# Optimization experiments

Measured on AMD Instinct MI355X. Metric: run time of the kernel, lower is better.

Reference implementation:

```python
import jax, jax.numpy as jnp
import numpy as np

N, E, F, FE, H, R = 100000, 3200000, 2, 7, 64, 500
BN_EPS = 1e-5
LEAKY_SLOPE = 0.01


def _bn(h, g, b):
    # BatchNorm1d in training mode: batch statistics over the node axis
    m = h.mean(0)
    v = h.var(0)
    return (h - m) * jax.lax.rsqrt(v + BN_EPS) * g + b


def _gine_conv(x, src, dst, edge_attr, eps, el_w, el_b, w1, b1, g, bt, w2, b2):
    # message: relu(x_j + Lin(edge_attr)); aggregate: scatter-add at dst
    msg = jax.nn.relu(x[src] + edge_attr @ el_w + el_b)          # [E, d]
    agg = jax.ops.segment_sum(msg, dst, num_segments=N)          # [N, d]
    h = (1.0 + eps) * x + agg
    # nn: Linear -> BN -> ReLU -> Linear -> ReLU
    h = jax.nn.relu(_bn(h @ w1 + b1, g, bt))
    return jax.nn.relu(h @ w2 + b2)


def setup_inputs() -> dict:
    key = jax.random.key(0)
    ks = jax.random.split(key, 16)
    r = lambda k, s, sc=0.1: jax.random.normal(k, s, dtype=jnp.float32) * sc
    return {
        "x": jax.random.normal(ks[0], (N, F), dtype=jnp.float32),
        "edge_attr": jax.random.normal(ks[1], (E, FE), dtype=jnp.float32),
        "edge_index": jax.random.randint(ks[2], (2, E), 0, N),
        "epoch": 1,
        "eps1": jnp.zeros((), jnp.float32),
        "el1_w": r(ks[3], (FE, F)), "el1_b": jnp.zeros((F,), jnp.float32),
        "n1_w1": r(ks[4], (F, H)), "n1_b1": jnp.zeros((H,), jnp.float32),
        "n1_g": jnp.ones((H,), jnp.float32), "n1_bt": jnp.zeros((H,), jnp.float32),
        "n1_w2": r(ks[5], (H, H)), "n1_b2": jnp.zeros((H,), jnp.float32),
        "eps2": jnp.zeros((), jnp.float32),
        "el2_w": r(ks[6], (FE, H)), "el2_b": jnp.zeros((H,), jnp.float32),
        "n2_w1": r(ks[7], (H, H)), "n2_b1": jnp.zeros((H,), jnp.float32),
        "n2_g": jnp.ones((H,), jnp.float32), "n2_bt": jnp.zeros((H,), jnp.float32),
        "n2_w2": r(ks[8], (H, H)), "n2_b2": jnp.zeros((H,), jnp.float32),
        "reg_w": r(ks[9], (H, R)), "reg_b": jnp.zeros((R,), jnp.float32),
        "end_w": r(ks[10], (R, 1)), "end_b": jnp.zeros((1,), jnp.float32),
    }


def reference(x, edge_attr, edge_index, epoch,
              eps1, el1_w, el1_b, n1_w1, n1_b1, n1_g, n1_bt, n1_w2, n1_b2,
              eps2, el2_w, el2_b, n2_w1, n2_b1, n2_g, n2_bt, n2_w2, n2_b2,
              reg_w, reg_b, end_w, end_b):
    src, dst = edge_index[0], edge_index[1]
    out = _gine_conv(x, src, dst, edge_attr, eps1, el1_w, el1_b,
                     n1_w1, n1_b1, n1_g, n1_bt, n1_w2, n1_b2)
    for _ in range(3 - 1):  # num_layers=3, shared conv2 weights
        out = _gine_conv(out, src, dst, edge_attr, eps2, el2_w, el2_b,
                         n2_w1, n2_b1, n2_g, n2_bt, n2_w2, n2_b2)
    # dropout p=0.0 -> identity; epoch only resets dropout, no effect here
    out = out @ reg_w + reg_b
    out = jnp.where(out >= 0, out, LEAKY_SLOPE * out)  # LeakyReLU
    out = out @ end_w + end_b                            # [N, 1]
    return out
```

## Files before the change

### kernel.cpp

```cpp
#include <hip/hip_runtime.h>
#include <hip/hip_fp16.h>

#define NN 100000
#define NE 3200000

__device__ inline unsigned pkh(float a, float b) {
  __half2 h;
  h.x = __float2half(a);
  h.y = __float2half(b);
  unsigned u;
  __builtin_memcpy(&u, &h, 4);
  return u;
}
__device__ inline float2 uph(unsigned u) {
  __half2 h;
  __builtin_memcpy(&h, &u, 4);
  return __half22float2(h);
}
__device__ inline float h1f(unsigned short v) {
  __half h;
  __builtin_memcpy(&h, &v, 2);
  return __half2float(h);
}
__device__ inline unsigned short f1h(float f) {
  __half h = __float2half(f);
  unsigned short u;
  __builtin_memcpy(&u, &h, 2);
  return u;
}

__global__ __launch_bounds__(256) void count_kernel(const int* __restrict__ dst,
                                                    int* __restrict__ cnt) {
  int stride = gridDim.x * 256;
  for (int e = blockIdx.x * 256 + threadIdx.x; e < NE; e += stride)
    atomicAdd(&cnt[dst[e]], 1);
}

__global__ __launch_bounds__(1024) void scan_kernel(const int* __restrict__ cnt,
                                                    int* __restrict__ rowptr,
                                                    int* __restrict__ ofs) {
  __shared__ int bsum[1024];
  int tid = threadIdx.x;
  const int CH = (NN + 1023) / 1024;
  int lo = tid * CH, hi = lo + CH < NN ? lo + CH : NN;
  if (lo > NN) lo = NN;
  if (hi < lo) hi = lo;
  int s = 0;
  for (int i = lo; i < hi; i++) s += cnt[i];
  bsum[tid] = s;
  __syncthreads();
  for (int off = 1; off < 1024; off <<= 1) {
    int v = bsum[tid];
    int u = (tid >= off) ? bsum[tid - off] : 0;
    __syncthreads();
    bsum[tid] = v + u;
    __syncthreads();
  }
  int pre = (tid == 0) ? 0 : bsum[tid - 1];
  for (int i = lo; i < hi; i++) {
    int cv = cnt[i];
    rowptr[i] = pre;
    ofs[i] = pre;
    pre += cv;
  }
  if (tid == 1023) rowptr[NN] = pre;
}

__global__ __launch_bounds__(256) void scatter2h_kernel(
    const int* __restrict__ src, const int* __restrict__ dst,
    const float* __restrict__ ea, int* __restrict__ ofs,
    uint4* __restrict__ erec, int* __restrict__ esrc,
    const float* __restrict__ x, const float* __restrict__ elw,
    const float* __restrict__ elb, float* __restrict__ msg1) {
  float w0[7], w1r[7];
#pragma unroll
  for (int k = 0; k < 7; k++) { w0[k] = elw[k * 2]; w1r[k] = elw[k * 2 + 1]; }
  float b0 = elb[0], b1 = elb[1];
  int stride = gridDim.x * 256;
  for (int e = blockIdx.x * 256 + threadIdx.x; e < NE; e += stride) {
    int sn = src[e];
    int pos = atomicAdd(&ofs[dst[e]], 1);
    float av[7];
#pragma unroll
    for (int k = 0; k < 7; k++) av[k] = ea[e * 7 + k];
    uint4 r;
    r.x = pkh(av[0], av[1]);
    r.y = pkh(av[2], av[3]);
    r.z = pkh(av[4], av[5]);
    r.w = pkh(av[6], 0.f);
    erec[pos] = r;
    esrc[pos] = sn;
    float m0 = b0, m1 = b1;
#pragma unroll
    for (int k = 0; k < 7; k++) {
      m0 = fmaf(av[k], w0[k], m0);
      m1 = fmaf(av[k], w1r[k], m1);
    }
    m0 = fmaxf(m0 + x[sn * 2 + 0], 0.f);
    m1 = fmaxf(m1 + x[sn * 2 + 1], 0.f);
    float2 mv; mv.x = m0; mv.y = m1;
    ((float2*)msg1)[pos] = mv;
  }
}

__global__ __launch_bounds__(256) void scatter1_kernel(
    const int* __restrict__ dst, int* __restrict__ ofs, int* __restrict__ eid_s) {
  int stride = gridDim.x * 256;
  for (int e = blockIdx.x * 256 + threadIdx.x; e < NE; e += stride) {
    int pos = atomicAdd(&ofs[dst[e]], 1);
    eid_s[pos] = e;
  }
}

__global__ __launch_bounds__(256) void l1sum_kernel(
    const int* __restrict__ rowptr, const float* __restrict__ msg1,
    float* __restrict__ agg) {
  int stride = gridDim.x * 256;
  for (int n = blockIdx.x * 256 + threadIdx.x; n < NN; n += stride) {
    int r0 = rowptr[n], r1 = rowptr[n + 1];
    float a0 = 0.f, a1 = 0.f;
    const float2* mp = (const float2*)msg1;
    for (int i = r0; i < r1; i++) {
      float2 v = mp[i];
      a0 += v.x;
      a1 += v.y;
    }
    agg[n * 2 + 0] = a0;
    agg[n * 2 + 1] = a1;
  }
}

__global__ __launch_bounds__(256) void l1agg_kernel(
    const int* __restrict__ rowptr, const int* __restrict__ eid_s,
    const int* __restrict__ src, const float* __restrict__ ea,
    const float* __restrict__ x, const float* __restrict__ elw,
    const float* __restrict__ elb, float* __restrict__ agg) {
  float w0[7], w1r[7];
#pragma unroll
  for (int k = 0; k < 7; k++) { w0[k] = elw[k * 2]; w1r[k] = elw[k * 2 + 1]; }
  float b0 = elb[0], b1 = elb[1];
  int stride = gridDim.x * 256;
  for (int n = blockIdx.x * 256 + threadIdx.x; n < NN; n += stride) {
    int r0 = rowptr[n], r1 = rowptr[n + 1];
    float a0 = 0.f, a1 = 0.f;
    for (int i = r0; i < r1; i++) {
      int e = eid_s[i];
      int sn = src[e];
      float m0 = b0, m1 = b1;
#pragma unroll
      for (int k = 0; k < 7; k++) {
        float a = ea[e * 7 + k];
        m0 = fmaf(a, w0[k], m0);
        m1 = fmaf(a, w1r[k], m1);
      }
      m0 = fmaxf(m0 + x[sn * 2 + 0], 0.f);
      m1 = fmaxf(m1 + x[sn * 2 + 1], 0.f);
      a0 += m0; a1 += m1;
    }
    agg[n * 2 + 0] = a0;
    agg[n * 2 + 1] = a1;
  }
}

#define PROJH(m, u) do { \
  float2 q0 = uph((u).x), q1 = uph((u).y), q2 = uph((u).z), q3 = uph((u).w); \
  m = bel; \
  m = fmaf(q0.x, wel[0], m); m = fmaf(q0.y, wel[1], m); \
  m = fmaf(q1.x, wel[2], m); m = fmaf(q1.y, wel[3], m); \
  m = fmaf(q2.x, wel[4], m); m = fmaf(q2.y, wel[5], m); \
  m = fmaf(q3.x, wel[6], m); } while (0)

__global__ __launch_bounds__(256) void gine64h_kernel(
    const int* __restrict__ rowptr, const uint4* __restrict__ erec,
    const int* __restrict__ esrc, const float* __restrict__ xin,
    const unsigned short* __restrict__ xh, const float* __restrict__ elw,
    const float* __restrict__ elb, const float* __restrict__ w1,
    const float* __restrict__ b1, const float* __restrict__ eps_p,
    float* __restrict__ tbuf, float* __restrict__ stats) {
  __shared__ float wl[64 * 64];
  __shared__ float hb[4][64];
  __shared__ float red[256];
  int tid = threadIdx.x, lane = tid & 63, wv = tid >> 6;
  for (int i2 = tid; i2 < 64 * 64; i2 += 256) wl[i2] = w1[i2];
  float wel[7];
#pragma unroll
  for (int k = 0; k < 7; k++) wel[k] = elw[k * 64 + lane];
  float bel = elb[lane], b1c = b1[lane];
  float ep = 1.0f + *eps_p;
  float s = 0.f, ss = 0.f;
  __syncthreads();
  const unsigned short* xl = xh + lane;
  int nw = gridDim.x * 4;
  for (int n = blockIdx.x * 4 + wv; n < NN; n += nw) {
    int r0 = rowptr[n], r1 = rowptr[n + 1];
    float acc = 0.f;
    int i = r0;
    int rem = r1 - r0;
    if (rem >= 4) {
      uint4 u0 = erec[i], u1 = erec[i + 1], u2 = erec[i + 2], u3 = erec[i + 3];
      int s0 = esrc[i], s1 = esrc[i + 1], s2 = esrc[i + 2], s3 = esrc[i + 3];
      while (true) {
        float g0 = h1f(xl[s0 * 64]);
        float g1 = h1f(xl[s1 * 64]);
        float g2 = h1f(xl[s2 * 64]);
        float g3 = h1f(xl[s3 * 64]);
        i += 4; rem -= 4;
        bool more = rem >= 4;
        int ip = more ? i : r0;
        uint4 v0 = erec[ip], v1 = erec[ip + 1], v2 = erec[ip + 2], v3 = erec[ip + 3];
        int t0 = esrc[ip], t1 = esrc[ip + 1], t2 = esrc[ip + 2], t3 = esrc[ip + 3];
        float m0, m1, m2, m3;
        PROJH(m0, u0); PROJH(m1, u1); PROJH(m2, u2); PROJH(m3, u3);
        acc += fmaxf(m0 + g0, 0.f);
        acc += fmaxf(m1 + g1, 0.f);
        acc += fmaxf(m2 + g2, 0.f);
        acc += fmaxf(m3 + g3, 0.f);
        u0 = v0; u1 = v1; u2 = v2; u3 = v3;
        s0 = t0; s1 = t1; s2 = t2; s3 = t3;
        if (!more) break;
      }
    }
    for (; i < r1; i++) {
      uint4 u = erec[i];
      int sn = esrc[i];
      float m;
      PROJH(m, u);
      m += h1f(xl[sn * 64]);
      acc += fmaxf(m, 0.f);
    }
    float h = ep * xin[n * 64 + lane] + acc;
    hb[wv][lane] = h;
    float t = b1c;
#pragma unroll
    for (int k = 0; k < 64; k++) t = fmaf(hb[wv][k], wl[k * 64 + lane], t);
    tbuf[n * 64 + lane] = t;
    s += t;
    ss += t * t;
  }
  double* dsum = (double*)stats;
  red[tid] = s;
  __syncthreads();
  if (tid < 64) unsafeAtomicAdd(&dsum[tid], (double)(red[tid] + red[tid + 64] + red[tid + 128] + red[tid + 192]));
  __syncthreads();
  red[tid] = ss;
  __syncthreads();
  if (tid < 64) unsafeAtomicAdd(&dsum[64 + tid], (double)(red[tid] + red[tid + 64] + red[tid + 128] + red[tid + 192]));
}

__global__ __launch_bounds__(256) void gine64s_kernel(
    const int* __restrict__ rowptr, const int* __restrict__ eid_s,
    const int* __restrict__ src, const float* __restrict__ ea,
    const float* __restrict__ xin, const float* __restrict__ elw,
    const float* __restrict__ elb, const float* __restrict__ w1,
    const float* __restrict__ b1, const float* __restrict__ eps_p,
    float* __restrict__ tbuf, float* __restrict__ stats) {
  __shared__ float wl[64 * 64];
  __shared__ float hb[4][64];
  __shared__ float red[256];
  int tid = threadIdx.x, lane = tid & 63, wv = tid >> 6;
  for (int i = tid; i < 64 * 64; i += 256) wl[i] = w1[i];
  float wel[7];
#pragma unroll
  for (int k = 0; k < 7; k++) wel[k] = elw[k * 64 + lane];
  float bel = elb[lane], b1c = b1[lane];
  float ep = 1.0f + *eps_p;
  float s = 0.f, ss = 0.f;
  __syncthreads();
  int nw = gridDim.x * 4;
  for (int n = blockIdx.x * 4 + wv; n < NN; n += nw) {
    int r0 = rowptr[n], r1 = rowptr[n + 1];
    float acc = 0.f;
    for (int i = r0; i < r1; i++) {
      int e = eid_s[i];
      int sn = src[e];
      float m = bel;
#pragma unroll
      for (int k = 0; k < 7; k++) m = fmaf(ea[e * 7 + k], wel[k], m);
      m += xin[sn * 64 + lane];
      acc += fmaxf(m, 0.f);
    }
    float h = ep * xin[n * 64 + lane] + acc;
    hb[wv][lane] = h;
    float t = b1c;
#pragma unroll
    for (int k = 0; k < 64; k++) t = fmaf(hb[wv][k], wl[k * 64 + lane], t);
    tbuf[n * 64 + lane] = t;
    s += t;
    ss += t * t;
  }
  double* dsum = (double*)stats;
  red[tid] = s;
  __syncthreads();
  if (tid < 64) unsafeAtomicAdd(&dsum[tid], (double)(red[tid] + red[tid + 64] + red[tid + 128] + red[tid + 192]));
  __syncthreads();
  red[tid] = ss;
  __syncthreads();
  if (tid < 64) unsafeAtomicAdd(&dsum[64 + tid], (double)(red[tid] + red[tid + 64] + red[tid + 128] + red[tid + 192]));
}

__global__ __launch_bounds__(256) void edge1_kernel(
    const float* __restrict__ x, const float* __restrict__ ea,
    const int* __restrict__ src, const int* __restrict__ dst,
    const float* __restrict__ elw, const float* __restrict__ elb,
    float* __restrict__ agg) {
  float w0[7], w1[7];
#pragma unroll
  for (int k = 0; k < 7; k++) { w0[k] = elw[k * 2]; w1[k] = elw[k * 2 + 1]; }
  float b0 = elb[0], b1 = elb[1];
  int stride = gridDim.x * 256;
  for (int e = blockIdx.x * 256 + threadIdx.x; e < NE; e += stride) {
    int s = src[e], d = dst[e];
    float m0 = b0, m1 = b1;
#pragma unroll
    for (int k = 0; k < 7; k++) {
      float a = ea[e * 7 + k];
      m0 = fmaf(a, w0[k], m0);
      m1 = fmaf(a, w1[k], m1);
    }
    m0 = fmaxf(m0 + x[s * 2 + 0], 0.f);
    m1 = fmaxf(m1 + x[s * 2 + 1], 0.f);
    unsafeAtomicAdd(&agg[d * 2 + 0], m0);
    unsafeAtomicAdd(&agg[d * 2 + 1], m1);
  }
}

__global__ __launch_bounds__(256) void edge64_kernel(
    const float* __restrict__ xin, const float* __restrict__ ea,
    const int* __restrict__ src, const int* __restrict__ dst,
    const float* __restrict__ elw, const float* __restrict__ elb,
    float* __restrict__ agg) {
  int lane = threadIdx.x & 63;
  int wid = (blockIdx.x * 256 + threadIdx.x) >> 6;
  int nw = (gridDim.x * 256) >> 6;
  float w[7];
#pragma unroll
  for (int k = 0; k < 7; k++) w[k] = elw[k * 64 + lane];
  float b = elb[lane];
  for (int e = wid; e < NE; e += nw) {
    int eu = __builtin_amdgcn_readfirstlane(e);
    int s = src[eu];
    int d = dst[eu];
    float m = b;
#pragma unroll
    for (int k = 0; k < 7; k++) m = fmaf(ea[eu * 7 + k], w[k], m);
    m += xin[s * 64 + lane];
    m = fmaxf(m, 0.f);
    unsafeAtomicAdd(&agg[d * 64 + lane], m);
  }
}

__global__ __launch_bounds__(256) void nodeA64_kernel(
    const float* __restrict__ xin, float* __restrict__ tbuf,
    const float* __restrict__ w1, const float* __restrict__ b1,
    const float* __restrict__ eps_p, float* __restrict__ stats) {
  __shared__ float wl[64 * 64];
  __shared__ float hbuf[4][64];
  __shared__ float red[256];
  int tid = threadIdx.x;
  int c = tid & 63, nl = tid >> 6;
  for (int i = tid; i < 64 * 64; i += 256) wl[i] = w1[i];
  float ep = 1.0f + *eps_p;
  float bc = b1[c];
  float s = 0.f, ss = 0.f;
  __syncthreads();
  for (int n0 = blockIdx.x * 4; n0 < NN; n0 += gridDim.x * 4) {
    int n = n0 + nl;
    bool valid = n < NN;
    float h = 0.f;
    if (valid) h = ep * xin[n * 64 + c] + tbuf[n * 64 + c];
    hbuf[nl][c] = h;
    __syncthreads();
    if (valid) {
      float t = bc;
#pragma unroll
      for (int k = 0; k < 64; k++) t = fmaf(hbuf[nl][k], wl[k * 64 + c], t);
      tbuf[n * 64 + c] = t;
      s += t;
      ss += t * t;
    }
    __syncthreads();
  }
  double* dsum = (double*)stats;
  red[tid] = s;
  __syncthreads();
  if (tid < 64) unsafeAtomicAdd(&dsum[tid], (double)(red[tid] + red[tid + 64] + red[tid + 128] + red[tid + 192]));
  __syncthreads();
  red[tid] = ss;
  __syncthreads();
  if (tid < 64) unsafeAtomicAdd(&dsum[64 + tid], (double)(red[tid] + red[tid + 64] + red[tid + 128] + red[tid + 192]));
}

__global__ __launch_bounds__(256) void nodeA2_kernel(
    const float* __restrict__ x, const float* __restrict__ agg1,
    float* __restrict__ tbuf, const float* __restrict__ w1,
    const float* __restrict__ b1, const float* __restrict__ eps_p,
    float* __restrict__ stats) {
  __shared__ float red[256];
  int tid = threadIdx.x;
  int c = tid & 63, nl = tid >> 6;
  float wa = w1[c], wb = w1[64 + c], bc = b1[c];
  float ep = 1.0f + *eps_p;
  float s = 0.f, ss = 0.f;
  for (int n0 = blockIdx.x * 4; n0 < NN; n0 += gridDim.x * 4) {
    int n = n0 + nl;
    if (n < NN) {
      float h0 = ep * x[n * 2 + 0] + agg1[n * 2 + 0];
      float h1 = ep * x[n * 2 + 1] + agg1[n * 2 + 1];
      float t = fmaf(h1, wb, fmaf(h0, wa, bc));
      tbuf[n * 64 + c] = t;
      s += t;
      ss += t * t;
    }
  }
  double* dsum = (double*)stats;
  red[tid] = s;
  __syncthreads();
  if (tid < 64) unsafeAtomicAdd(&dsum[tid], (double)(red[tid] + red[tid + 64] + red[tid + 128] + red[tid + 192]));
  __syncthreads();
  red[tid] = ss;
  __syncthreads();
  if (tid < 64) unsafeAtomicAdd(&dsum[64 + tid], (double)(red[tid] + red[tid + 64] + red[tid + 128] + red[tid + 192]));
}

__global__ __launch_bounds__(256) void nodeB_kernel(
    const float* __restrict__ tin, float* __restrict__ outb,
    const float* __restrict__ w2, const float* __restrict__ b2,
    const float* __restrict__ stats, const float* __restrict__ g,
    const float* __restrict__ bt, unsigned short* __restrict__ xh) {
  __shared__ float wl[64 * 64];
  __shared__ float ubuf[4][64];
  __shared__ float scsh[128];
  int tid = threadIdx.x;
  int c = tid & 63, nl = tid >> 6;
  for (int i = tid; i < 64 * 64; i += 256) wl[i] = w2[i];
  if (tid < 64) {
    const double* ds = (const double*)stats;
    double m = ds[tid] / (double)NN;
    double v = ds[64 + tid] / (double)NN - m * m;
    float sc = g[tid] * (float)(1.0 / sqrt(v + 1e-5));
    scsh[tid] = sc;
    scsh[64 + tid] = bt[tid] - (float)m * sc;
  }
  float bc = b2[c];
  __syncthreads();
  float scale = scsh[c], shift = scsh[64 + c];
  for (int n0 = blockIdx.x * 4; n0 < NN; n0 += gridDim.x * 4) {
    int n = n0 + nl;
    bool valid = n < NN;
    float u = 0.f;
    if (valid) {
      float t = tin[n * 64 + c];
      u = fmaxf(fmaf(t, scale, shift), 0.f);
    }
    ubuf[nl][c] = u;
    __syncthreads();
    if (valid) {
      float o = bc;
#pragma unroll
      for (int k = 0; k < 64; k++) o = fmaf(ubuf[nl][k], wl[k * 64 + c], o);
      o = fmaxf(o, 0.f);
      outb[n * 64 + c] = o;
      if (xh) xh[n * 64 + c] = f1h(o);
    }
    __syncthreads();
  }
}

__global__ __launch_bounds__(256) void final_kernel(
    const float* __restrict__ xin, const float* __restrict__ regw,
    const float* __restrict__ regb, const float* __restrict__ endw,
    const float* __restrict__ endb, float* __restrict__ out) {
  __shared__ float wl[64 * 128];
  __shared__ float eb[256];
  int tid = threadIdx.x;
  int node = blockIdx.x * 256 + tid;
  bool valid = node < NN;
  float xr[64];
  if (valid) {
    const float4* xp = (const float4*)(xin + node * 64);
#pragma unroll
    for (int k4 = 0; k4 < 16; k4++) {
      float4 v = xp[k4];
      xr[k4 * 4 + 0] = v.x; xr[k4 * 4 + 1] = v.y;
      xr[k4 * 4 + 2] = v.z; xr[k4 * 4 + 3] = v.w;
    }
  }
  float y = 0.f;
  for (int ch = 0; ch < 4; ch++) {
    int j0 = ch * 125;
    __syncthreads();
    for (int idx = tid; idx < 64 * 125; idx += 256) {
      int k = idx / 125;
      int jl = idx - k * 125;
      wl[k * 128 + jl] = regw[k * 500 + j0 + jl];
    }
    if (tid < 125) { eb[tid] = regb[j0 + tid]; eb[128 + tid] = endw[j0 + tid]; }
    __syncthreads();
    if (valid) {
      int jl = 0;
      for (; jl + 4 <= 125; jl += 4) {
        float t0 = eb[jl], t1 = eb[jl + 1], t2 = eb[jl + 2], t3 = eb[jl + 3];
#pragma unroll
        for (int k = 0; k < 64; k++) {
          float4 w4 = *(const float4*)&wl[k * 128 + jl];
          float xv = xr[k];
          t0 = fmaf(xv, w4.x, t0);
          t1 = fmaf(xv, w4.y, t1);
          t2 = fmaf(xv, w4.z, t2);
          t3 = fmaf(xv, w4.w, t3);
        }
        t0 = t0 >= 0.f ? t0 : 0.01f * t0;
        t1 = t1 >= 0.f ? t1 : 0.01f * t1;
        t2 = t2 >= 0.f ? t2 : 0.01f * t2;
        t3 = t3 >= 0.f ? t3 : 0.01f * t3;
        y += t0 * eb[128 + jl] + t1 * eb[128 + jl + 1] + t2 * eb[128 + jl + 2] + t3 * eb[128 + jl + 3];
      }
      {
        float t = eb[124];
#pragma unroll
        for (int k = 0; k < 64; k++) t = fmaf(xr[k], wl[k * 128 + 124], t);
        t = t >= 0.f ? t : 0.01f * t;
        y += t * eb[128 + 124];
      }
    }
  }
  if (valid) out[node] = y + endb[0];
}

extern "C" void kernel_launch(void* const* d_in, const int* in_sizes, int n_in,
                              void* d_out, int out_size, void* d_ws, size_t ws_size,
                              hipStream_t stream) {
  const float* x    = (const float*)d_in[0];
  const float* ea   = (const float*)d_in[1];
  const int*   ei   = (const int*)d_in[2];
  const float* eps1 = (const float*)d_in[4];
  const float* el1w = (const float*)d_in[5];
  const float* el1b = (const float*)d_in[6];
  const float* n1w1 = (const float*)d_in[7];
  const float* n1b1 = (const float*)d_in[8];
  const float* n1g  = (const float*)d_in[9];
  const float* n1bt = (const float*)d_in[10];
  const float* n1w2 = (const float*)d_in[11];
  const float* n1b2 = (const float*)d_in[12];
  const float* eps2 = (const float*)d_in[13];
  const float* el2w = (const float*)d_in[14];
  const float* el2b = (const float*)d_in[15];
  const float* n2w1 = (const float*)d_in[16];
  const float* n2b1 = (const float*)d_in[17];
  const float* n2g  = (const float*)d_in[18];
  const float* n2bt = (const float*)d_in[19];
  const float* n2w2 = (const float*)d_in[20];
  const float* n2b2 = (const float*)d_in[21];
  const float* regw = (const float*)d_in[22];
  const float* regb = (const float*)d_in[23];
  const float* endw = (const float*)d_in[24];
  const float* endb = (const float*)d_in[25];
  const int* srcp = ei;
  const int* dstp = ei + NE;

  const size_t o_stats  = 0;
  const size_t o_cnt    = 768;
  const size_t o_rowptr = 100768;
  const size_t o_buf0   = 200832;
  const size_t o_buf1   = 6600832;
  const size_t o_xh     = 13000832;
  const size_t o_agg1   = 16200832;
  const size_t o_edat   = 16400832;
  const size_t o_srcs   = 29200832;
  const size_t needA2 = (o_srcs + (size_t)NE) * 4;
  const size_t needA1 = (o_edat + (size_t)NE) * 4;
  const size_t needB  = (2 * 6600000 + 384) * 4;

  float* wsf = (float*)d_ws;

  if (ws_size >= needA1) {
    const bool packed = ws_size >= needA2;
    float* stats0 = wsf + o_stats;
    float* stats1 = wsf + o_stats + 256;
    float* stats2 = wsf + o_stats + 512;
    int* cnt     = (int*)(wsf + o_cnt);
    int* rowptr  = (int*)(wsf + o_rowptr);
    float* buf0  = wsf + o_buf0;
    float* buf1  = wsf + o_buf1;
    unsigned short* xh = (unsigned short*)(wsf + o_xh);
    float* agg1  = wsf + o_agg1;
    uint4* erec  = (uint4*)(wsf + o_edat);
    int* esrc    = (int*)(wsf + o_srcs);
    float* msg1  = buf0;

    hipMemsetAsync(wsf, 0, (768 + NN) * sizeof(float), stream);

    count_kernel<<<4096, 256, 0, stream>>>(dstp, cnt);
    scan_kernel<<<1, 1024, 0, stream>>>(cnt, rowptr, cnt);
    if (packed)
      scatter2h_kernel<<<4096, 256, 0, stream>>>(srcp, dstp, ea, cnt, erec, esrc,
                                                 x, el1w, el1b, msg1);
    else
      scatter1_kernel<<<4096, 256, 0, stream>>>(dstp, cnt, (int*)(wsf + o_edat));

    if (packed)
      l1sum_kernel<<<391, 256, 0, stream>>>(rowptr, msg1, agg1);
    else
      l1agg_kernel<<<391, 256, 0, stream>>>(rowptr, (const int*)(wsf + o_edat),
                                            srcp, ea, x, el1w, el1b, agg1);
    nodeA2_kernel<<<2048, 256, 0, stream>>>(x, agg1, buf1, n1w1, n1b1, eps1, stats0);
    nodeB_kernel<<<2048, 256, 0, stream>>>(buf1, buf1, n1w2, n1b2, stats0,
                                           n1g, n1bt, packed ? xh : nullptr);

    if (packed) {
      gine64h_kernel<<<4096, 256, 0, stream>>>(rowptr, erec, esrc, buf1, xh,
                                               el2w, el2b, n2w1, n2b1, eps2,
                                               buf0, stats1);
      nodeB_kernel<<<2048, 256, 0, stream>>>(buf0, buf0, n2w2, n2b2, stats1,
                                             n2g, n2bt, xh);
      gine64h_kernel<<<4096, 256, 0, stream>>>(rowptr, erec, esrc, buf0, xh,
                                               el2w, el2b, n2w1, n2b1, eps2,
                                               buf1, stats2);
      nodeB_kernel<<<2048, 256, 0, stream>>>(buf1, buf1, n2w2, n2b2, stats2,
                                             n2g, n2bt, nullptr);
      final_kernel<<<(NN + 255) / 256, 256, 0, stream>>>(buf1, regw, regb, endw,
                                                         endb, (float*)d_out);
    } else {
      float* cur = buf1;
      float* wrk = buf0;
      float* sl[2] = {stats1, stats2};
      for (int l = 0; l < 2; l++) {
        gine64s_kernel<<<4096, 256, 0, stream>>>(rowptr, (const int*)(wsf + o_edat),
                                                 srcp, ea, cur, el2w, el2b, n2w1,
                                                 n2b1, eps2, wrk, sl[l]);
        nodeB_kernel<<<2048, 256, 0, stream>>>(wrk, wrk, n2w2, n2b2, sl[l],
                                               n2g, n2bt, nullptr);
        float* tmp = cur; cur = wrk; wrk = tmp;
      }
      final_kernel<<<(NN + 255) / 256, 256, 0, stream>>>(cur, regw, regb, endw,
                                                         endb, (float*)d_out);
    }
    return;
  }

  if (ws_size < needB) return;
  const size_t BUF = 6600000;
  float* buf0 = (float*)d_ws;
  float* buf1 = buf0 + BUF;
  float* stats = buf1 + BUF;

  float* t1 = buf1;
  float* agg1 = buf1 + NN * 64;
  hipMemsetAsync(agg1, 0, NN * 2 * sizeof(float), stream);
  hipMemsetAsync(stats, 0, 128 * sizeof(double), stream);
  edge1_kernel<<<2048, 256, 0, stream>>>(x, ea, srcp, dstp, el1w, el1b, agg1);
  nodeA2_kernel<<<2048, 256, 0, stream>>>(x, agg1, t1, n1w1, n1b1, eps1, stats);
  nodeB_kernel<<<2048, 256, 0, stream>>>(t1, buf1, n1w2, n1b2, stats, n1g, n1bt,
                                         nullptr);

  float* cur = buf1;
  float* wrk = buf0;
  for (int l = 0; l < 2; l++) {
    hipMemsetAsync(wrk, 0, NN * 64 * sizeof(float), stream);
    hipMemsetAsync(stats, 0, 128 * sizeof(double), stream);
    edge64_kernel<<<2048, 256, 0, stream>>>(cur, ea, srcp, dstp, el2w, el2b, wrk);
    nodeA64_kernel<<<2048, 256, 0, stream>>>(cur, wrk, n2w1, n2b1, eps2, stats);
    nodeB_kernel<<<2048, 256, 0, stream>>>(wrk, wrk, n2w2, n2b2, stats, n2g, n2bt,
                                           nullptr);
    float* tmp = cur; cur = wrk; wrk = tmp;
  }

  final_kernel<<<(NN + 255) / 256, 256, 0, stream>>>(cur, regw, regb, endw, endb,
                                                     (float*)d_out);
}
```

Measured before the change: 1.346 ms.

## Two-pass binned CSR sort with fused layer-1 aggregation via atomics

Replaces the single random-scatter edge sort with a two-pass scheme. Edges are first scattered into coarse bins of 128 destination nodes into a packed staging buffer, with the source id split across spare half bits and a byte array. A per-bin kernel then does the fine scatter inside a small, cache-friendly region and accumulates the layer-1 messages straight into agg1 with float atomics, which removes the msg1 buffer and the l1sum pass. This adds an extra pass over the edge data and float atomics, so the layer-1 sums become order-dependent, and the packing relies on node ids fitting in 17 bits.

```diff
diff --git a/kernel.cpp b/kernel.cpp
--- a/kernel.cpp
+++ b/kernel.cpp
@@ -3,6 +3,7 @@
 
 #define NN 100000
 #define NE 3200000
+#define NBINS 782
 
 __device__ inline unsigned pkh(float a, float b) {
   __half2 h;
@@ -66,40 +67,72 @@
   if (tid == 1023) rowptr[NN] = pre;
 }
 
-__global__ __launch_bounds__(256) void scatter2h_kernel(
+__global__ __launch_bounds__(1024) void binit_kernel(const int* __restrict__ rowptr,
+                                                     int* __restrict__ binofs) {
+  int t = threadIdx.x;
+  if (t < NBINS) binofs[t] = rowptr[t * 128];
+}
+
+__global__ __launch_bounds__(256) void binscat_kernel(
     const int* __restrict__ src, const int* __restrict__ dst,
-    const float* __restrict__ ea, int* __restrict__ ofs,
-    uint4* __restrict__ erec, int* __restrict__ esrc,
-    const float* __restrict__ x, const float* __restrict__ elw,
-    const float* __restrict__ elb, float* __restrict__ msg1) {
-  float w0[7], w1r[7];
-#pragma unroll
-  for (int k = 0; k < 7; k++) { w0[k] = elw[k * 2]; w1r[k] = elw[k * 2 + 1]; }
-  float b0 = elb[0], b1 = elb[1];
+    const float* __restrict__ ea, int* __restrict__ binofs,
+    uint4* __restrict__ stageA, unsigned char* __restrict__ stageB) {
   int stride = gridDim.x * 256;
   for (int e = blockIdx.x * 256 + threadIdx.x; e < NE; e += stride) {
     int sn = src[e];
-    int pos = atomicAdd(&ofs[dst[e]], 1);
+    int dn = dst[e];
+    int pos = atomicAdd(&binofs[dn >> 7], 1);
     float av[7];
 #pragma unroll
     for (int k = 0; k < 7; k++) av[k] = ea[e * 7 + k];
+    unsigned extra = ((unsigned)(dn & 127) << 9) | ((unsigned)sn >> 8);
     uint4 r;
     r.x = pkh(av[0], av[1]);
     r.y = pkh(av[2], av[3]);
     r.z = pkh(av[4], av[5]);
-    r.w = pkh(av[6], 0.f);
-    erec[pos] = r;
+    r.w = (unsigned)f1h(av[6]) | (extra << 16);
+    stageA[pos] = r;
+    stageB[pos] = (unsigned char)(sn & 255);
+  }
+}
+
+__global__ __launch_bounds__(256) void binsort_kernel(
+    const int* __restrict__ rowptr, const uint4* __restrict__ stageA,
+    const unsigned char* __restrict__ stageB, int* __restrict__ ofs,
+    uint4* __restrict__ erec, int* __restrict__ esrc,
+    const float* __restrict__ x, const float* __restrict__ elw,
+    const float* __restrict__ elb, float* __restrict__ agg1) {
+  float w0[7], w1r[7];
+#pragma unroll
+  for (int k = 0; k < 7; k++) { w0[k] = elw[k * 2]; w1r[k] = elw[k * 2 + 1]; }
+  float b0 = elb[0], b1 = elb[1];
+  int b = blockIdx.x;
+  int nhi = (b + 1) * 128;
+  if (nhi > NN) nhi = NN;
+  int r0 = rowptr[b * 128], r1 = rowptr[nhi];
+  int base = b << 7;
+  for (int i = r0 + threadIdx.x; i < r1; i += 256) {
+    uint4 u = stageA[i];
+    unsigned extra = u.w >> 16;
+    int sn = (int)(((extra & 0x1FF) << 8) | (unsigned)stageB[i]);
+    int dn = base + (int)(extra >> 9);
+    int pos = atomicAdd(&ofs[dn], 1);
+    erec[pos] = u;
     esrc[pos] = sn;
+    float2 q0 = uph(u.x), q1 = uph(u.y), q2 = uph(u.z);
+    float e6 = h1f((unsigned short)(u.w & 0xFFFF));
     float m0 = b0, m1 = b1;
-#pragma unroll
-    for (int k = 0; k < 7; k++) {
-      m0 = fmaf(av[k], w0[k], m0);
-      m1 = fmaf(av[k], w1r[k], m1);
-    }
+    m0 = fmaf(q0.x, w0[0], m0); m1 = fmaf(q0.x, w1r[0], m1);
+    m0 = fmaf(q0.y, w0[1], m0); m1 = fmaf(q0.y, w1r[1], m1);
+    m0 = fmaf(q1.x, w0[2], m0); m1 = fmaf(q1.x, w1r[2], m1);
+    m0 = fmaf(q1.y, w0[3], m0); m1 = fmaf(q1.y, w1r[3], m1);
+    m0 = fmaf(q2.x, w0[4], m0); m1 = fmaf(q2.x, w1r[4], m1);
+    m0 = fmaf(q2.y, w0[5], m0); m1 = fmaf(q2.y, w1r[5], m1);
+    m0 = fmaf(e6, w0[6], m0);   m1 = fmaf(e6, w1r[6], m1);
     m0 = fmaxf(m0 + x[sn * 2 + 0], 0.f);
     m1 = fmaxf(m1 + x[sn * 2 + 1], 0.f);
-    float2 mv; mv.x = m0; mv.y = m1;
-    ((float2*)msg1)[pos] = mv;
+    unsafeAtomicAdd(&agg1[dn * 2 + 0], m0);
+    unsafeAtomicAdd(&agg1[dn * 2 + 1], m1);
   }
 }
 
@@ -109,24 +142,6 @@
   for (int e = blockIdx.x * 256 + threadIdx.x; e < NE; e += stride) {
     int pos = atomicAdd(&ofs[dst[e]], 1);
     eid_s[pos] = e;
-  }
-}
-
-__global__ __launch_bounds__(256) void l1sum_kernel(
-    const int* __restrict__ rowptr, const float* __restrict__ msg1,
-    float* __restrict__ agg) {
-  int stride = gridDim.x * 256;
-  for (int n = blockIdx.x * 256 + threadIdx.x; n < NN; n += stride) {
-    int r0 = rowptr[n], r1 = rowptr[n + 1];
-    float a0 = 0.f, a1 = 0.f;
-    const float2* mp = (const float2*)msg1;
-    for (int i = r0; i < r1; i++) {
-      float2 v = mp[i];
-      a0 += v.x;
-      a1 += v.y;
-    }
-    agg[n * 2 + 0] = a0;
-    agg[n * 2 + 1] = a1;
   }
 }
 
@@ -559,16 +574,17 @@
   const int* dstp = ei + NE;
 
   const size_t o_stats  = 0;
-  const size_t o_cnt    = 768;
-  const size_t o_rowptr = 100768;
-  const size_t o_buf0   = 200832;
-  const size_t o_buf1   = 6600832;
-  const size_t o_xh     = 13000832;
-  const size_t o_agg1   = 16200832;
-  const size_t o_edat   = 16400832;
-  const size_t o_srcs   = 29200832;
-  const size_t needA2 = (o_srcs + (size_t)NE) * 4;
-  const size_t needA1 = (o_edat + (size_t)NE) * 4;
+  const size_t o_agg1   = 768;
+  const size_t o_cnt    = 200768;
+  const size_t o_binofs = 300768;
+  const size_t o_rowptr = 301568;
+  const size_t o_buf0   = 401600;
+  const size_t o_buf1   = 6801600;
+  const size_t o_xh     = 13201600;
+  const size_t o_erec   = 16401600;
+  const size_t o_esrc   = 29201600;
+  const size_t needA2 = (o_esrc + (size_t)NE) * 4;
+  const size_t needA1 = (o_erec + (size_t)NE) * 4;
   const size_t needB  = (2 * 6600000 + 384) * 4;
 
   float* wsf = (float*)d_ws;
@@ -578,31 +594,34 @@
     float* stats0 = wsf + o_stats;
     float* stats1 = wsf + o_stats + 256;
     float* stats2 = wsf + o_stats + 512;
+    float* agg1  = wsf + o_agg1;
     int* cnt     = (int*)(wsf + o_cnt);
+    int* binofs  = (int*)(wsf + o_binofs);
     int* rowptr  = (int*)(wsf + o_rowptr);
     float* buf0  = wsf + o_buf0;
     float* buf1  = wsf + o_buf1;
     unsigned short* xh = (unsigned short*)(wsf + o_xh);
-    float* agg1  = wsf + o_agg1;
-    uint4* erec  = (uint4*)(wsf + o_edat);
-    int* esrc    = (int*)(wsf + o_srcs);
-    float* msg1  = buf0;
-
-    hipMemsetAsync(wsf, 0, (768 + NN) * sizeof(float), stream);
+    uint4* erec  = (uint4*)(wsf + o_erec);
+    int* esrc    = (int*)(wsf + o_esrc);
+    uint4* stageA = (uint4*)(wsf + o_buf0);
+    unsigned char* stageB = (unsigned char*)(wsf + o_xh);
+
+    hipMemsetAsync(wsf, 0, (o_binofs) * sizeof(float), stream);
 
     count_kernel<<<4096, 256, 0, stream>>>(dstp, cnt);
     scan_kernel<<<1, 1024, 0, stream>>>(cnt, rowptr, cnt);
-    if (packed)
-      scatter2h_kernel<<<4096, 256, 0, stream>>>(srcp, dstp, ea, cnt, erec, esrc,
-                                                 x, el1w, el1b, msg1);
-    else
-      scatter1_kernel<<<4096, 256, 0, stream>>>(dstp, cnt, (int*)(wsf + o_edat));
-
-    if (packed)
-      l1sum_kernel<<<391, 256, 0, stream>>>(rowptr, msg1, agg1);
-    else
-      l1agg_kernel<<<391, 256, 0, stream>>>(rowptr, (const int*)(wsf + o_edat),
+    if (packed) {
+      binit_kernel<<<1, 1024, 0, stream>>>(rowptr, binofs);
+      binscat_kernel<<<4096, 256, 0, stream>>>(srcp, dstp, ea, binofs,
+                                               stageA, stageB);
+      binsort_kernel<<<NBINS, 256, 0, stream>>>(rowptr, stageA, stageB, cnt,
+                                                erec, esrc, x, el1w, el1b, agg1);
+    } else {
+      scatter1_kernel<<<4096, 256, 0, stream>>>(dstp, cnt, (int*)(wsf + o_erec));
+      l1agg_kernel<<<391, 256, 0, stream>>>(rowptr, (const int*)(wsf + o_erec),
                                             srcp, ea, x, el1w, el1b, agg1);
+    }
+
     nodeA2_kernel<<<2048, 256, 0, stream>>>(x, agg1, buf1, n1w1, n1b1, eps1, stats0);
     nodeB_kernel<<<2048, 256, 0, stream>>>(buf1, buf1, n1w2, n1b2, stats0,
                                            n1g, n1bt, packed ? xh : nullptr);
@@ -625,7 +644,7 @@
       float* wrk = buf0;
       float* sl[2] = {stats1, stats2};
       for (int l = 0; l < 2; l++) {
-        gine64s_kernel<<<4096, 256, 0, stream>>>(rowptr, (const int*)(wsf + o_edat),
+        gine64s_kernel<<<4096, 256, 0, stream>>>(rowptr, (const int*)(wsf + o_erec),
                                                  srcp, ea, cur, el2w, el2b, n2w1,
                                                  n2b1, eps2, wrk, sl[l]);
         nodeB_kernel<<<2048, 256, 0, stream>>>(wrk, wrk, n2w2, n2b2, sl[l],
```

Measured after the change: 2.164 ms. 60.7% more time.

## Pack source index into edge record and fuse layer-1 aggregation via atomics

Applied to the files above, without the earlier changes.

The 17-bit source node index is now packed into the spare half of the last word of each 16-byte edge record, taking the low mantissa bit of the seventh attribute. This removes the separate esrc array and its loads in both 64-wide GINE layers. Layer-1 messages are now atomically added straight into agg1 in the scatter kernel, which drops the msg1 buffer and the l1sum pass. The cost is float atomic contention on 200k addresses, a nondeterministic summation order, and a tiny precision loss in edge attribute 6.

```diff
diff --git a/kernel.cpp b/kernel.cpp
--- a/kernel.cpp
+++ b/kernel.cpp
@@ -66,12 +66,12 @@
   if (tid == 1023) rowptr[NN] = pre;
 }
 
-__global__ __launch_bounds__(256) void scatter2h_kernel(
+__global__ __launch_bounds__(256) void scatter2c_kernel(
     const int* __restrict__ src, const int* __restrict__ dst,
     const float* __restrict__ ea, int* __restrict__ ofs,
-    uint4* __restrict__ erec, int* __restrict__ esrc,
-    const float* __restrict__ x, const float* __restrict__ elw,
-    const float* __restrict__ elb, float* __restrict__ msg1) {
+    uint4* __restrict__ erec, const float* __restrict__ x,
+    const float* __restrict__ elw, const float* __restrict__ elb,
+    float* __restrict__ agg1) {
   float w0[7], w1r[7];
 #pragma unroll
   for (int k = 0; k < 7; k++) { w0[k] = elw[k * 2]; w1r[k] = elw[k * 2 + 1]; }
@@ -79,7 +79,8 @@
   int stride = gridDim.x * 256;
   for (int e = blockIdx.x * 256 + threadIdx.x; e < NE; e += stride) {
     int sn = src[e];
-    int pos = atomicAdd(&ofs[dst[e]], 1);
+    int dn = dst[e];
+    int pos = atomicAdd(&ofs[dn], 1);
     float av[7];
 #pragma unroll
     for (int k = 0; k < 7; k++) av[k] = ea[e * 7 + k];
@@ -87,9 +88,9 @@
     r.x = pkh(av[0], av[1]);
     r.y = pkh(av[2], av[3]);
     r.z = pkh(av[4], av[5]);
-    r.w = pkh(av[6], 0.f);
+    r.w = ((unsigned)f1h(av[6]) & 0xFFFEu) | ((unsigned)sn >> 16) |
+          (((unsigned)sn & 0xFFFFu) << 16);
     erec[pos] = r;
-    esrc[pos] = sn;
     float m0 = b0, m1 = b1;
 #pragma unroll
     for (int k = 0; k < 7; k++) {
@@ -98,8 +99,8 @@
     }
     m0 = fmaxf(m0 + x[sn * 2 + 0], 0.f);
     m1 = fmaxf(m1 + x[sn * 2 + 1], 0.f);
-    float2 mv; mv.x = m0; mv.y = m1;
-    ((float2*)msg1)[pos] = mv;
+    unsafeAtomicAdd(&agg1[dn * 2 + 0], m0);
+    unsafeAtomicAdd(&agg1[dn * 2 + 1], m1);
   }
 }
 
@@ -109,24 +110,6 @@
   for (int e = blockIdx.x * 256 + threadIdx.x; e < NE; e += stride) {
     int pos = atomicAdd(&ofs[dst[e]], 1);
     eid_s[pos] = e;
-  }
-}
-
-__global__ __launch_bounds__(256) void l1sum_kernel(
-    const int* __restrict__ rowptr, const float* __restrict__ msg1,
-    float* __restrict__ agg) {
-  int stride = gridDim.x * 256;
-  for (int n = blockIdx.x * 256 + threadIdx.x; n < NN; n += stride) {
-    int r0 = rowptr[n], r1 = rowptr[n + 1];
-    float a0 = 0.f, a1 = 0.f;
-    const float2* mp = (const float2*)msg1;
-    for (int i = r0; i < r1; i++) {
-      float2 v = mp[i];
-      a0 += v.x;
-      a1 += v.y;
-    }
-    agg[n * 2 + 0] = a0;
-    agg[n * 2 + 1] = a1;
   }
 }
 
@@ -162,21 +145,24 @@
   }
 }
 
-#define PROJH(m, u) do { \
-  float2 q0 = uph((u).x), q1 = uph((u).y), q2 = uph((u).z), q3 = uph((u).w); \
+#define PROJH2(m, u) do { \
+  float2 q0 = uph((u).x), q1 = uph((u).y), q2 = uph((u).z); \
+  float e6 = h1f((unsigned short)((u).w & 0xFFFEu)); \
   m = bel; \
   m = fmaf(q0.x, wel[0], m); m = fmaf(q0.y, wel[1], m); \
   m = fmaf(q1.x, wel[2], m); m = fmaf(q1.y, wel[3], m); \
   m = fmaf(q2.x, wel[4], m); m = fmaf(q2.y, wel[5], m); \
-  m = fmaf(q3.x, wel[6], m); } while (0)
+  m = fmaf(e6, wel[6], m); } while (0)
+
+#define SRCOF(u) ((int)((((u).w & 1u) << 16) | ((u).w >> 16)))
 
 __global__ __launch_bounds__(256) void gine64h_kernel(
     const int* __restrict__ rowptr, const uint4* __restrict__ erec,
-    const int* __restrict__ esrc, const float* __restrict__ xin,
-    const unsigned short* __restrict__ xh, const float* __restrict__ elw,
-    const float* __restrict__ elb, const float* __restrict__ w1,
-    const float* __restrict__ b1, const float* __restrict__ eps_p,
-    float* __restrict__ tbuf, float* __restrict__ stats) {
+    const float* __restrict__ xin, const unsigned short* __restrict__ xh,
+    const float* __restrict__ elw, const float* __restrict__ elb,
+    const float* __restrict__ w1, const float* __restrict__ b1,
+    const float* __restrict__ eps_p, float* __restrict__ tbuf,
+    float* __restrict__ stats) {
   __shared__ float wl[64 * 64];
   __shared__ float hb[4][64];
   __shared__ float red[256];
@@ -198,8 +184,8 @@
     int rem = r1 - r0;
     if (rem >= 4) {
       uint4 u0 = erec[i], u1 = erec[i + 1], u2 = erec[i + 2], u3 = erec[i + 3];
-      int s0 = esrc[i], s1 = esrc[i + 1], s2 = esrc[i + 2], s3 = esrc[i + 3];
       while (true) {
+        int s0 = SRCOF(u0), s1 = SRCOF(u1), s2 = SRCOF(u2), s3 = SRCOF(u3);
         float g0 = h1f(xl[s0 * 64]);
         float g1 = h1f(xl[s1 * 64]);
         float g2 = h1f(xl[s2 * 64]);
@@ -208,23 +194,21 @@
         bool more = rem >= 4;
         int ip = more ? i : r0;
         uint4 v0 = erec[ip], v1 = erec[ip + 1], v2 = erec[ip + 2], v3 = erec[ip + 3];
-        int t0 = esrc[ip], t1 = esrc[ip + 1], t2 = esrc[ip + 2], t3 = esrc[ip + 3];
         float m0, m1, m2, m3;
-        PROJH(m0, u0); PROJH(m1, u1); PROJH(m2, u2); PROJH(m3, u3);
+        PROJH2(m0, u0); PROJH2(m1, u1); PROJH2(m2, u2); PROJH2(m3, u3);
         acc += fmaxf(m0 + g0, 0.f);
         acc += fmaxf(m1 + g1, 0.f);
         acc += fmaxf(m2 + g2, 0.f);
         acc += fmaxf(m3 + g3, 0.f);
         u0 = v0; u1 = v1; u2 = v2; u3 = v3;
-        s0 = t0; s1 = t1; s2 = t2; s3 = t3;
         if (!more) break;
       }
     }
     for (; i < r1; i++) {
       uint4 u = erec[i];
-      int sn = esrc[i];
+      int sn = SRCOF(u);
       float m;
-      PROJH(m, u);
+      PROJH2(m, u);
       m += h1f(xl[sn * 64]);
       acc += fmaxf(m, 0.f);
     }
@@ -559,16 +543,15 @@
   const int* dstp = ei + NE;
 
   const size_t o_stats  = 0;
-  const size_t o_cnt    = 768;
-  const size_t o_rowptr = 100768;
-  const size_t o_buf0   = 200832;
-  const size_t o_buf1   = 6600832;
-  const size_t o_xh     = 13000832;
-  const size_t o_agg1   = 16200832;
-  const size_t o_edat   = 16400832;
-  const size_t o_srcs   = 29200832;
-  const size_t needA2 = (o_srcs + (size_t)NE) * 4;
-  const size_t needA1 = (o_edat + (size_t)NE) * 4;
+  const size_t o_agg1   = 768;
+  const size_t o_cnt    = 200768;
+  const size_t o_rowptr = 300768;
+  const size_t o_buf0   = 400832;
+  const size_t o_buf1   = 6800832;
+  const size_t o_xh     = 13200832;
+  const size_t o_erec   = 16400832;
+  const size_t needA2 = (o_erec + (size_t)NE * 4) * 4;
+  const size_t needA1 = (o_erec + (size_t)NE) * 4;
   const size_t needB  = (2 * 6600000 + 384) * 4;
 
   float* wsf = (float*)d_ws;
@@ -578,42 +561,38 @@
     float* stats0 = wsf + o_stats;
     float* stats1 = wsf + o_stats + 256;
     float* stats2 = wsf + o_stats + 512;
+    float* agg1  = wsf + o_agg1;
     int* cnt     = (int*)(wsf + o_cnt);
     int* rowptr  = (int*)(wsf + o_rowptr);
     float* buf0  = wsf + o_buf0;
     float* buf1  = wsf + o_buf1;
     unsigned short* xh = (unsigned short*)(wsf + o_xh);
-    float* agg1  = wsf + o_agg1;
-    uint4* erec  = (uint4*)(wsf + o_edat);
-    int* esrc    = (int*)(wsf + o_srcs);
-    float* msg1  = buf0;
-
-    hipMemsetAsync(wsf, 0, (768 + NN) * sizeof(float), stream);
+    uint4* erec  = (uint4*)(wsf + o_erec);
+
+    hipMemsetAsync(wsf, 0, o_rowptr * sizeof(float), stream);
 
     count_kernel<<<4096, 256, 0, stream>>>(dstp, cnt);
     scan_kernel<<<1, 1024, 0, stream>>>(cnt, rowptr, cnt);
     if (packed)
-      scatter2h_kernel<<<4096, 256, 0, stream>>>(srcp, dstp, ea, cnt, erec, esrc,
-                                                 x, el1w, el1b, msg1);
-    else
-      scatter1_kernel<<<4096, 256, 0, stream>>>(dstp, cnt, (int*)(wsf + o_edat));
-
-    if (packed)
-      l1sum_kernel<<<391, 256, 0, stream>>>(rowptr, msg1, agg1);
-    else
-      l1agg_kernel<<<391, 256, 0, stream>>>(rowptr, (const int*)(wsf + o_edat),
+      scatter2c_kernel<<<4096, 256, 0, stream>>>(srcp, dstp, ea, cnt, erec,
+                                                 x, el1w, el1b, agg1);
+    else {
+      scatter1_kernel<<<4096, 256, 0, stream>>>(dstp, cnt, (int*)(wsf + o_erec));
+      l1agg_kernel<<<391, 256, 0, stream>>>(rowptr, (const int*)(wsf + o_erec),
                                             srcp, ea, x, el1w, el1b, agg1);
+    }
+
     nodeA2_kernel<<<2048, 256, 0, stream>>>(x, agg1, buf1, n1w1, n1b1, eps1, stats0);
     nodeB_kernel<<<2048, 256, 0, stream>>>(buf1, buf1, n1w2, n1b2, stats0,
                                            n1g, n1bt, packed ? xh : nullptr);
 
     if (packed) {
-      gine64h_kernel<<<4096, 256, 0, stream>>>(rowptr, erec, esrc, buf1, xh,
+      gine64h_kernel<<<4096, 256, 0, stream>>>(rowptr, erec, buf1, xh,
                                                el2w, el2b, n2w1, n2b1, eps2,
                                                buf0, stats1);
       nodeB_kernel<<<2048, 256, 0, stream>>>(buf0, buf0, n2w2, n2b2, stats1,
                                              n2g, n2bt, xh);
-      gine64h_kernel<<<4096, 256, 0, stream>>>(rowptr, erec, esrc, buf0, xh,
+      gine64h_kernel<<<4096, 256, 0, stream>>>(rowptr, erec, buf0, xh,
                                                el2w, el2b, n2w1, n2b1, eps2,
                                                buf1, stats2);
       nodeB_kernel<<<2048, 256, 0, stream>>>(buf1, buf1, n2w2, n2b2, stats2,
@@ -625,7 +604,7 @@
       float* wrk = buf0;
       float* sl[2] = {stats1, stats2};
       for (int l = 0; l < 2; l++) {
-        gine64s_kernel<<<4096, 256, 0, stream>>>(rowptr, (const int*)(wsf + o_edat),
+        gine64s_kernel<<<4096, 256, 0, stream>>>(rowptr, (const int*)(wsf + o_erec),
                                                  srcp, ea, cur, el2w, el2b, n2w1,
                                                  n2b1, eps2, wrk, sl[l]);
         nodeB_kernel<<<2048, 256, 0, stream>>>(wrk, wrk, n2w2, n2b2, sl[l],
```

Result: slower. 1.590 ms (+18.2%).
